# Optimization experiments

Measured on AMD Instinct MI355X. Metric: run time of the kernel, lower is better.

## Reference

```python
import jax, jax.numpy as jnp
import numpy as np

B, N, K, C = 8, 4096, 32, 128
HEAD_DIM = 64          # out_channels(512) // num_heads(8)
POS_DIM = HEAD_DIM // 2
D_THRESHOLD = 0.04


def setup_inputs() -> dict:
    key = jax.random.key(0)
    ks = jax.random.split(key, 16)

    def W(k, fi, fo):
        return (jax.random.normal(k, (fi, fo), jnp.float32) / np.sqrt(fi)).astype(jnp.float32)

    return {
        "center_xyz": jax.random.normal(ks[0], (B, N, 3), jnp.float32),
        "center_features": jax.random.normal(ks[1], (B, N, C), jnp.float32),
        "neighbor_xyz": jax.random.normal(ks[2], (B, N, K, 3), jnp.float32),
        "neighbor_features": jax.random.normal(ks[3], (B, N, K, C), jnp.float32),
        "phi_w": W(ks[4], C, HEAD_DIM),   "phi_b": jnp.zeros((HEAD_DIM,), jnp.float32),
        "theta_w": W(ks[5], C, HEAD_DIM), "theta_b": jnp.zeros((HEAD_DIM,), jnp.float32),
        "m1_w": W(ks[6], 3, POS_DIM),     "m1_b": jnp.zeros((POS_DIM,), jnp.float32),
        "m2_w": W(ks[7], 3, POS_DIM),     "m2_b": jnp.zeros((POS_DIM,), jnp.float32),
        "psi_w": W(ks[8], 2 * POS_DIM, 1), "psi_b": jnp.zeros((1,), jnp.float32),
        "z_w": W(ks[9], C, HEAD_DIM),     "z_b": jnp.zeros((HEAD_DIM,), jnp.float32),
    }


def reference(center_xyz, center_features, neighbor_xyz, neighbor_features,
              phi_w, phi_b, theta_w, theta_b, m1_w, m1_b, m2_w, m2_b,
              psi_w, psi_b, z_w, z_b):
    relu = jax.nn.relu
    # feature affinity r_f: (B,N,K,1)
    feat_i = relu(center_features @ phi_w + phi_b)        # (B,N,H)
    feat_j = relu(neighbor_features @ theta_w + theta_b)  # (B,N,K,H)
    r_f = jnp.sum(feat_i[:, :, None, :] * feat_j, axis=-1, keepdims=True)
    # positional score r_l_base: (B,N,K,1)
    pos_i = relu(center_xyz @ m1_w + m1_b)                # (B,N,P)
    pos_j = relu(neighbor_xyz @ m2_w + m2_b)              # (B,N,K,P)
    pos_i_t = jnp.broadcast_to(pos_i[:, :, None, :], pos_j.shape)
    r_l_base = relu(jnp.concatenate([pos_i_t, pos_j], axis=-1) @ psi_w + psi_b)
    # SPIL mask: same frame (z coord equal) AND distance > threshold
    t_i = center_xyz[..., 2][:, :, None]                  # (B,N,1)
    t_j = neighbor_xyz[..., 2]                            # (B,N,K)
    same_frame = (t_i == t_j).astype(jnp.float32)
    euclid = jnp.linalg.norm(center_xyz[:, :, None, :] - neighbor_xyz, axis=-1)
    dist_mask = (euclid > D_THRESHOLD).astype(jnp.float32)
    mask = same_frame * dist_mask                         # (B,N,K)
    r_l = r_l_base * (1.0 - mask[..., None])
    # masked, r_l-weighted softmax over K
    r_f = r_f / jnp.sqrt(jnp.float32(HEAD_DIM))
    r_f_max = jnp.max(r_f, axis=2, keepdims=True)
    numerator = r_l * jnp.exp(r_f - r_f_max)
    denominator = jnp.sum(numerator, axis=2, keepdims=True) + 1e-8
    W_ij = numerator / denominator                        # (B,N,K,1)
    transformed = neighbor_features @ z_w + z_b           # (B,N,K,H)
    return jnp.sum(W_ij * transformed, axis=2)            # (B,N,H)
```

## Files before the change

### kernel.cpp

```cpp
#include <hip/hip_runtime.h>
#include <hip/hip_bf16.h>


#define Bq 8
#define Nq 4096
#define Kq 32
#define Cq 128
#define Hq 64

typedef __bf16 bf16x8 __attribute__((ext_vector_type(8)));
typedef float  f32x4  __attribute__((ext_vector_type(4)));

__device__ __forceinline__ unsigned short f2bf(float f) {
  __hip_bfloat16 h = __float2bfloat16(f);
  return *reinterpret_cast<unsigned short*>(&h);
}
__device__ __forceinline__ float bf2f(unsigned short u) {
  return __uint_as_float(((unsigned int)u) << 16);
}

__global__ __launch_bounds__(256) void prep_w(const float* __restrict__ theta_w,
                                              const float* __restrict__ z_w,
                                              const float* __restrict__ phi_w,
                                              unsigned short* __restrict__ WcT,
                                              unsigned short* __restrict__ phiT) {
  int idx = blockIdx.x * 256 + threadIdx.x;
  if (idx < 16384) {
    int h = idx >> 7, c = idx & 127;
    float v = (h < 64) ? theta_w[c * 64 + h] : z_w[c * 64 + (h - 64)];
    WcT[idx] = f2bf(v);
  } else {
    int i2 = idx - 16384;
    int h = i2 >> 7, c = i2 & 127;
    phiT[i2] = f2bf(phi_w[c * 64 + h]);
  }
}

__global__ __launch_bounds__(256) void phi_gemm(
    const float* __restrict__ cf, const float* __restrict__ cxyz,
    const unsigned short* __restrict__ phiT, const float* __restrict__ phi_b,
    const float* __restrict__ m1_w, const float* __restrict__ m1_b,
    const float* __restrict__ psi_w,
    float* __restrict__ feat_out, float* __restrict__ s_out) {
  __shared__ __align__(16) unsigned short Xs[128 * 128];
  const int t = threadIdx.x;
  const int wave = t >> 6, lane = t & 63;
  const int lo16 = lane & 15, quad = lane >> 4;
  const size_t n0 = (size_t)blockIdx.x * 128;

  bf16x8 wf[4][4];
#pragma unroll
  for (int ks = 0; ks < 4; ks++)
#pragma unroll
    for (int nt = 0; nt < 4; nt++)
      wf[ks][nt] = *(const bf16x8*)(phiT + (size_t)(nt * 16 + lo16) * 128 + ks * 32 + quad * 8);

  const float4* xsrc = (const float4*)(cf + n0 * Cq);
  ushort4* xdst4 = (ushort4*)Xs;
#pragma unroll
  for (int i = 0; i < 16; i++) {
    int j = t + i * 256;
    float4 v = xsrc[j];
    int r = j >> 5, w = j & 31;
    int g = w >> 1, hf = w & 1;
    int p = g ^ (r & 15);
    ushort4 pk;
    pk.x = f2bf(v.x); pk.y = f2bf(v.y); pk.z = f2bf(v.z); pk.w = f2bf(v.w);
    xdst4[r * 32 + p * 2 + hf] = pk;
  }
  __syncthreads();

  f32x4 acc[2][4];
#pragma unroll
  for (int mt = 0; mt < 2; mt++)
#pragma unroll
    for (int nt = 0; nt < 4; nt++) acc[mt][nt] = (f32x4){0.f, 0.f, 0.f, 0.f};
#pragma unroll
  for (int ks = 0; ks < 4; ks++) {
    int p = (ks * 4 + quad) ^ lo16;
    bf16x8 a[2];
#pragma unroll
    for (int mt = 0; mt < 2; mt++) {
      int row = wave * 32 + mt * 16 + lo16;
      a[mt] = *(const bf16x8*)(Xs + row * 128 + p * 8);
    }
#pragma unroll
    for (int mt = 0; mt < 2; mt++)
#pragma unroll
      for (int nt = 0; nt < 4; nt++)
        acc[mt][nt] = __builtin_amdgcn_mfma_f32_16x16x32_bf16(a[mt], wf[ks][nt], acc[mt][nt], 0, 0, 0);
  }

#pragma unroll
  for (int mt = 0; mt < 2; mt++)
#pragma unroll
    for (int nt = 0; nt < 4; nt++) {
      int h = nt * 16 + lo16;
      float b = phi_b[h];
#pragma unroll
      for (int r = 0; r < 4; r++) {
        int row = wave * 32 + mt * 16 + quad * 4 + r;
        feat_out[(n0 + row) * 64 + h] = fmaxf(acc[mt][nt][r] + b, 0.f);
      }
    }

  if (t < 128) {
    size_t n = n0 + t;
    float x = cxyz[n * 3], y = cxyz[n * 3 + 1], z = cxyz[n * 3 + 2];
    float s = 0.f;
#pragma unroll 4
    for (int p = 0; p < 32; p++) {
      float pi = fmaxf(fmaf(x, m1_w[p], fmaf(y, m1_w[32 + p], fmaf(z, m1_w[64 + p], m1_b[p]))), 0.f);
      s = fmaf(pi, psi_w[p], s);
    }
    s_out[n] = s;
  }
}

__global__ __launch_bounds__(256, 3) void spil_main(
    const float* __restrict__ cxyz, const float* __restrict__ nxyz,
    const float* __restrict__ nf,
    const float* __restrict__ theta_b, const float* __restrict__ m2_w,
    const float* __restrict__ m2_b, const float* __restrict__ psi_w,
    const float* __restrict__ psi_b, const float* __restrict__ z_b,
    const unsigned short* __restrict__ WcT,
    const float* __restrict__ feat_i, const float* __restrict__ s_i,
    float* __restrict__ out) {
  __shared__ __align__(16) char smem[35968];
  unsigned short* Xs   = (unsigned short*)smem;
  unsigned short* outt = (unsigned short*)smem;
  float* feat_s = (float*)(smem + 33792);
  float* m2w_s  = feat_s + 256;
  float* m2b_s  = m2w_s + 96;
  float* psij_s = m2b_s + 32;
  float* zb_s   = psij_s + 32;
  float* tb_s   = zb_s + 64;

  const int t = threadIdx.x;
  const int wave = t >> 6, lane = t & 63;
  const int lo16 = lane & 15, quad = lane >> 4;
  const size_t n0 = (size_t)blockIdx.x * 4;

  const int mhalf = wave & 1, nhalf = wave >> 1;
  bf16x8 wf[4][4];
#pragma unroll
  for (int ks = 0; ks < 4; ks++)
#pragma unroll
    for (int nt = 0; nt < 4; nt++)
      wf[ks][nt] = *(const bf16x8*)(WcT + (size_t)(nhalf * 64 + nt * 16 + lo16) * 128 + ks * 32 + quad * 8);

  const float4* xsrc = (const float4*)(nf + n0 * Kq * Cq);
  ushort4* xdst4 = (ushort4*)Xs;
#pragma unroll
  for (int i = 0; i < 16; i++) {
    int j = t + i * 256;
    float4 v = xsrc[j];
    int r = j >> 5, w = j & 31;
    int g = w >> 1, hf = w & 1;
    int p = g ^ (r & 15);
    ushort4 pk;
    pk.x = f2bf(v.x); pk.y = f2bf(v.y); pk.z = f2bf(v.z); pk.w = f2bf(v.w);
    xdst4[r * 32 + p * 2 + hf] = pk;
  }
  __syncthreads();

  f32x4 acc[4][4];
#pragma unroll
  for (int mt = 0; mt < 4; mt++)
#pragma unroll
    for (int nt = 0; nt < 4; nt++) acc[mt][nt] = (f32x4){0.f, 0.f, 0.f, 0.f};
#pragma unroll
  for (int ks = 0; ks < 4; ks++) {
    int p = (ks * 4 + quad) ^ lo16;
    bf16x8 a[4];
#pragma unroll
    for (int mt = 0; mt < 4; mt++) {
      int row = mhalf * 64 + mt * 16 + lo16;
      a[mt] = *(const bf16x8*)(Xs + row * 128 + p * 8);
    }
#pragma unroll
    for (int mt = 0; mt < 4; mt++)
#pragma unroll
      for (int nt = 0; nt < 4; nt++)
        acc[mt][nt] = __builtin_amdgcn_mfma_f32_16x16x32_bf16(a[mt], wf[ks][nt], acc[mt][nt], 0, 0, 0);
  }
  __syncthreads();

#pragma unroll
  for (int mt = 0; mt < 4; mt++) {
    int row0 = mhalf * 64 + mt * 16 + quad * 4;
#pragma unroll
    for (int nt = 0; nt < 4; nt++) {
      int col = nhalf * 64 + nt * 16 + lo16;
#pragma unroll
      for (int r = 0; r < 4; r++)
        outt[(row0 + r) * 132 + col] = f2bf(acc[mt][nt][r]);
    }
  }
  feat_s[t] = feat_i[n0 * 64 + t];
  if (t < 96) m2w_s[t] = m2_w[t];
  if (t < 32) { m2b_s[t] = m2_b[t]; psij_s[t] = psi_w[32 + t]; }
  if (t < 64) { zb_s[t] = z_b[t]; tb_s[t] = theta_b[t]; }
  __syncthreads();

  const int nl = wave;
  const size_t ng = n0 + nl;
  const int k = lane & 31, half = lane >> 5;
  const int baser = nl * 32;

  const float* fi = feat_s + nl * 64;
  const unsigned short* orow = outt + (size_t)(baser + k) * 132;
  float v = 0.f;
#pragma unroll
  for (int i = 0; i < 32; i++) {
    int h = half * 32 + i;
    float fj = fmaxf(bf2f(orow[h]) + tb_s[h], 0.f);
    v = fmaf(fj, fi[h], v);
  }
  v += __shfl_xor(v, 32);
  float r_f = v * 0.125f;

  float cx = cxyz[ng * 3 + 0], cy = cxyz[ng * 3 + 1], cz = cxyz[ng * 3 + 2];
  const float* nxp = nxyz + (ng * Kq + (size_t)k) * 3;
  float xj = nxp[0], yj = nxp[1], zj = nxp[2];
  float sj = 0.f;
#pragma unroll
  for (int p = 0; p < 32; p++) {
    float pj = fmaxf(fmaf(xj, m2w_s[p], fmaf(yj, m2w_s[32 + p], fmaf(zj, m2w_s[64 + p], m2b_s[p]))), 0.f);
    sj = fmaf(pj, psij_s[p], sj);
  }
  float rl = fmaxf(s_i[ng] + sj + psi_b[0], 0.f);
  float dx = cx - xj, dy = cy - yj, dz = cz - zj;
  float dist = sqrtf(dx * dx + dy * dy + dz * dz);
  if (cz == zj && dist > 0.04f) rl = 0.f;

  float m = r_f;
#pragma unroll
  for (int off = 16; off; off >>= 1) m = fmaxf(m, __shfl_xor(m, off));
  float e = rl * __expf(r_f - m);
  float s = e;
#pragma unroll
  for (int off = 16; off; off >>= 1) s += __shfl_xor(s, off);
  float wgt = e / (s + 1e-8f);

  const int h = lane;
  const float zb = zb_s[h];
  float o = 0.f;
#pragma unroll
  for (int kk = 0; kk < 32; kk++) {
    float w = __shfl(wgt, kk);
    o = fmaf(w, bf2f(outt[(baser + kk) * 132 + 64 + h]) + zb, o);
  }
  out[ng * 64 + h] = o;
}

extern "C" void kernel_launch(void* const* d_in, const int* in_sizes, int n_in,
                              void* d_out, int out_size, void* d_ws, size_t ws_size,
                              hipStream_t stream) {
  const float* cxyz    = (const float*)d_in[0];
  const float* cf      = (const float*)d_in[1];
  const float* nxyz    = (const float*)d_in[2];
  const float* nf      = (const float*)d_in[3];
  const float* phi_w   = (const float*)d_in[4];
  const float* phi_b   = (const float*)d_in[5];
  const float* theta_w = (const float*)d_in[6];
  const float* theta_b = (const float*)d_in[7];
  const float* m1_w    = (const float*)d_in[8];
  const float* m1_b    = (const float*)d_in[9];
  const float* m2_w    = (const float*)d_in[10];
  const float* m2_b    = (const float*)d_in[11];
  const float* psi_w   = (const float*)d_in[12];
  const float* psi_b   = (const float*)d_in[13];
  const float* z_w     = (const float*)d_in[14];
  const float* z_b     = (const float*)d_in[15];
  float* outp = (float*)d_out;

  char* ws = (char*)d_ws;
  unsigned short* WcT  = (unsigned short*)ws;
  unsigned short* phiT = (unsigned short*)(ws + 32768);
  float* feat = (float*)(ws + 49152);
  float* s_i  = (float*)(ws + 49152 + (size_t)Bq * Nq * 64 * 4);

  prep_w<<<96, 256, 0, stream>>>(theta_w, z_w, phi_w, WcT, phiT);
  phi_gemm<<<(Bq * Nq) / 128, 256, 0, stream>>>(cf, cxyz, phiT, phi_b, m1_w, m1_b, psi_w, feat, s_i);
  spil_main<<<(Bq * Nq) / 4, 256, 0, stream>>>(cxyz, nxyz, nf, theta_b, m2_w, m2_b, psi_w, psi_b,
                                               z_b, WcT, feat, s_i, outp);
}
```

Before: 741.6 us.

## Make spil_main persistent over 8 tiles with double-buffered LDS prefetch

Each block now processes eight 4-point tiles in a loop instead of one. The weight fragments are loaded once per block, and the next tile's neighbor features are read from global into registers while the current tile's MFMA runs, then written into an alternate LDS buffer. This aims to hide global load latency and amortize the per-block weight loads. The costs are doubled LDS use (about 70KB), lower occupancy (launch bounds 2 instead of 3), higher register pressure from holding 16 prefetched ushort4 values, and a grid of only 1024 blocks.

```diff
diff --git a/kernel.cpp b/kernel.cpp
--- a/kernel.cpp
+++ b/kernel.cpp
@@ -7,6 +7,7 @@
 #define Kq 32
 #define Cq 128
 #define Hq 64
+#define TILES 8
 
 typedef __bf16 bf16x8 __attribute__((ext_vector_type(8)));
 typedef float  f32x4  __attribute__((ext_vector_type(4)));
@@ -117,7 +118,7 @@
   }
 }
 
-__global__ __launch_bounds__(256, 3) void spil_main(
+__global__ __launch_bounds__(256, 2) void spil_main(
     const float* __restrict__ cxyz, const float* __restrict__ nxyz,
     const float* __restrict__ nf,
     const float* __restrict__ theta_b, const float* __restrict__ m2_w,
@@ -126,11 +127,9 @@
     const unsigned short* __restrict__ WcT,
     const float* __restrict__ feat_i, const float* __restrict__ s_i,
     float* __restrict__ out) {
-  __shared__ __align__(16) char smem[35968];
-  unsigned short* Xs   = (unsigned short*)smem;
-  unsigned short* outt = (unsigned short*)smem;
-  float* feat_s = (float*)(smem + 33792);
-  float* m2w_s  = feat_s + 256;
+  __shared__ __align__(16) char smem[70784];
+  float* feat_d = (float*)(smem + 67584);
+  float* m2w_s  = feat_d + 512;
   float* m2b_s  = m2w_s + 96;
   float* psij_s = m2b_s + 32;
   float* zb_s   = psij_s + 32;
@@ -139,9 +138,9 @@
   const int t = threadIdx.x;
   const int wave = t >> 6, lane = t & 63;
   const int lo16 = lane & 15, quad = lane >> 4;
-  const size_t n0 = (size_t)blockIdx.x * 4;
-
   const int mhalf = wave & 1, nhalf = wave >> 1;
+  const size_t g0 = (size_t)blockIdx.x * TILES;
+
   bf16x8 wf[4][4];
 #pragma unroll
   for (int ks = 0; ks < 4; ks++)
@@ -149,109 +148,145 @@
     for (int nt = 0; nt < 4; nt++)
       wf[ks][nt] = *(const bf16x8*)(WcT + (size_t)(nhalf * 64 + nt * 16 + lo16) * 128 + ks * 32 + quad * 8);
 
-  const float4* xsrc = (const float4*)(nf + n0 * Kq * Cq);
-  ushort4* xdst4 = (ushort4*)Xs;
-#pragma unroll
-  for (int i = 0; i < 16; i++) {
-    int j = t + i * 256;
-    float4 v = xsrc[j];
-    int r = j >> 5, w = j & 31;
-    int g = w >> 1, hf = w & 1;
-    int p = g ^ (r & 15);
-    ushort4 pk;
-    pk.x = f2bf(v.x); pk.y = f2bf(v.y); pk.z = f2bf(v.z); pk.w = f2bf(v.w);
-    xdst4[r * 32 + p * 2 + hf] = pk;
-  }
-  __syncthreads();
-
-  f32x4 acc[4][4];
-#pragma unroll
-  for (int mt = 0; mt < 4; mt++)
-#pragma unroll
-    for (int nt = 0; nt < 4; nt++) acc[mt][nt] = (f32x4){0.f, 0.f, 0.f, 0.f};
-#pragma unroll
-  for (int ks = 0; ks < 4; ks++) {
-    int p = (ks * 4 + quad) ^ lo16;
-    bf16x8 a[4];
-#pragma unroll
-    for (int mt = 0; mt < 4; mt++) {
-      int row = mhalf * 64 + mt * 16 + lo16;
-      a[mt] = *(const bf16x8*)(Xs + row * 128 + p * 8);
-    }
-#pragma unroll
-    for (int mt = 0; mt < 4; mt++)
-#pragma unroll
-      for (int nt = 0; nt < 4; nt++)
-        acc[mt][nt] = __builtin_amdgcn_mfma_f32_16x16x32_bf16(a[mt], wf[ks][nt], acc[mt][nt], 0, 0, 0);
-  }
-  __syncthreads();
-
-#pragma unroll
-  for (int mt = 0; mt < 4; mt++) {
-    int row0 = mhalf * 64 + mt * 16 + quad * 4;
-#pragma unroll
-    for (int nt = 0; nt < 4; nt++) {
-      int col = nhalf * 64 + nt * 16 + lo16;
-#pragma unroll
-      for (int r = 0; r < 4; r++)
-        outt[(row0 + r) * 132 + col] = f2bf(acc[mt][nt][r]);
-    }
-  }
-  feat_s[t] = feat_i[n0 * 64 + t];
   if (t < 96) m2w_s[t] = m2_w[t];
   if (t < 32) { m2b_s[t] = m2_b[t]; psij_s[t] = psi_w[32 + t]; }
   if (t < 64) { zb_s[t] = z_b[t]; tb_s[t] = theta_b[t]; }
+
+  {
+    const float4* xsrc = (const float4*)(nf + g0 * 4 * Kq * Cq);
+    ushort4* xd = (ushort4*)smem;
+#pragma unroll
+    for (int i = 0; i < 16; i++) {
+      int j = t + i * 256;
+      float4 v = xsrc[j];
+      int r = j >> 5, w = j & 31;
+      int g = w >> 1, hf = w & 1;
+      int p = g ^ (r & 15);
+      ushort4 pk;
+      pk.x = f2bf(v.x); pk.y = f2bf(v.y); pk.z = f2bf(v.z); pk.w = f2bf(v.w);
+      xd[r * 32 + p * 2 + hf] = pk;
+    }
+    feat_d[t] = feat_i[g0 * 256 + t];
+  }
   __syncthreads();
 
-  const int nl = wave;
-  const size_t ng = n0 + nl;
-  const int k = lane & 31, half = lane >> 5;
-  const int baser = nl * 32;
-
-  const float* fi = feat_s + nl * 64;
-  const unsigned short* orow = outt + (size_t)(baser + k) * 132;
-  float v = 0.f;
-#pragma unroll
-  for (int i = 0; i < 32; i++) {
-    int h = half * 32 + i;
-    float fj = fmaxf(bf2f(orow[h]) + tb_s[h], 0.f);
-    v = fmaf(fj, fi[h], v);
-  }
-  v += __shfl_xor(v, 32);
-  float r_f = v * 0.125f;
-
-  float cx = cxyz[ng * 3 + 0], cy = cxyz[ng * 3 + 1], cz = cxyz[ng * 3 + 2];
-  const float* nxp = nxyz + (ng * Kq + (size_t)k) * 3;
-  float xj = nxp[0], yj = nxp[1], zj = nxp[2];
-  float sj = 0.f;
-#pragma unroll
-  for (int p = 0; p < 32; p++) {
-    float pj = fmaxf(fmaf(xj, m2w_s[p], fmaf(yj, m2w_s[32 + p], fmaf(zj, m2w_s[64 + p], m2b_s[p]))), 0.f);
-    sj = fmaf(pj, psij_s[p], sj);
-  }
-  float rl = fmaxf(s_i[ng] + sj + psi_b[0], 0.f);
-  float dx = cx - xj, dy = cy - yj, dz = cz - zj;
-  float dist = sqrtf(dx * dx + dy * dy + dz * dz);
-  if (cz == zj && dist > 0.04f) rl = 0.f;
-
-  float m = r_f;
-#pragma unroll
-  for (int off = 16; off; off >>= 1) m = fmaxf(m, __shfl_xor(m, off));
-  float e = rl * __expf(r_f - m);
-  float s = e;
-#pragma unroll
-  for (int off = 16; off; off >>= 1) s += __shfl_xor(s, off);
-  float wgt = e / (s + 1e-8f);
-
-  const int h = lane;
-  const float zb = zb_s[h];
-  float o = 0.f;
-#pragma unroll
-  for (int kk = 0; kk < 32; kk++) {
-    float w = __shfl(wgt, kk);
-    o = fmaf(w, bf2f(outt[(baser + kk) * 132 + 64 + h]) + zb, o);
-  }
-  out[ng * 64 + h] = o;
+  int cur = 0;
+  for (int it = 0; it < TILES; ++it) {
+    const size_t gtile = g0 + it;
+    const size_t n0 = gtile * 4;
+    const bool more = (it + 1 < TILES);
+
+    ushort4 pk[16];
+    if (more) {
+      const float4* xsrc = (const float4*)(nf + (n0 + 4) * Kq * Cq);
+#pragma unroll
+      for (int i = 0; i < 16; i++) {
+        float4 v = xsrc[t + i * 256];
+        pk[i].x = f2bf(v.x); pk[i].y = f2bf(v.y); pk[i].z = f2bf(v.z); pk[i].w = f2bf(v.w);
+      }
+    }
+
+    const size_t ng = n0 + wave;
+    const int k = lane & 31, half = lane >> 5;
+    const float* nxp = nxyz + (ng * Kq + (size_t)k) * 3;
+    const float xj = nxp[0], yj = nxp[1], zj = nxp[2];
+    const float cx = cxyz[ng * 3], cy = cxyz[ng * 3 + 1], cz = cxyz[ng * 3 + 2];
+    const float sI = s_i[ng];
+
+    const unsigned short* Xs = (const unsigned short*)(smem + cur * 33792);
+    f32x4 acc[4][4];
+#pragma unroll
+    for (int mt = 0; mt < 4; mt++)
+#pragma unroll
+      for (int nt = 0; nt < 4; nt++) acc[mt][nt] = (f32x4){0.f, 0.f, 0.f, 0.f};
+#pragma unroll
+    for (int ks = 0; ks < 4; ks++) {
+      int p = (ks * 4 + quad) ^ lo16;
+      bf16x8 a[4];
+#pragma unroll
+      for (int mt = 0; mt < 4; mt++) {
+        int row = mhalf * 64 + mt * 16 + lo16;
+        a[mt] = *(const bf16x8*)(Xs + row * 128 + p * 8);
+      }
+#pragma unroll
+      for (int mt = 0; mt < 4; mt++)
+#pragma unroll
+        for (int nt = 0; nt < 4; nt++)
+          acc[mt][nt] = __builtin_amdgcn_mfma_f32_16x16x32_bf16(a[mt], wf[ks][nt], acc[mt][nt], 0, 0, 0);
+    }
+    __syncthreads();
+
+    unsigned short* outt = (unsigned short*)(smem + cur * 33792);
+#pragma unroll
+    for (int mt = 0; mt < 4; mt++) {
+      int row0 = mhalf * 64 + mt * 16 + quad * 4;
+#pragma unroll
+      for (int nt = 0; nt < 4; nt++) {
+        int col = nhalf * 64 + nt * 16 + lo16;
+#pragma unroll
+        for (int r = 0; r < 4; r++)
+          outt[(row0 + r) * 132 + col] = f2bf(acc[mt][nt][r]);
+      }
+    }
+
+    if (more) {
+      ushort4* xd = (ushort4*)(smem + (cur ^ 1) * 33792);
+#pragma unroll
+      for (int i = 0; i < 16; i++) {
+        int j = t + i * 256;
+        int r = j >> 5, w = j & 31;
+        int g = w >> 1, hf = w & 1;
+        int p = g ^ (r & 15);
+        xd[r * 32 + p * 2 + hf] = pk[i];
+      }
+      feat_d[(cur ^ 1) * 256 + t] = feat_i[(gtile + 1) * 256 + t];
+    }
+    __syncthreads();
+
+    const float* fi = feat_d + cur * 256 + wave * 64;
+    const unsigned short* orow = outt + (size_t)(wave * 32 + k) * 132;
+    float vv = 0.f;
+#pragma unroll
+    for (int i = 0; i < 32; i++) {
+      int h = half * 32 + i;
+      float fj = fmaxf(bf2f(orow[h]) + tb_s[h], 0.f);
+      vv = fmaf(fj, fi[h], vv);
+    }
+    vv += __shfl_xor(vv, 32);
+    float r_f = vv * 0.125f;
+
+    float sj = 0.f;
+#pragma unroll
+    for (int p = 0; p < 32; p++) {
+      float pj = fmaxf(fmaf(xj, m2w_s[p], fmaf(yj, m2w_s[32 + p], fmaf(zj, m2w_s[64 + p], m2b_s[p]))), 0.f);
+      sj = fmaf(pj, psij_s[p], sj);
+    }
+    float rl = fmaxf(sI + sj + psi_b[0], 0.f);
+    float dx = cx - xj, dy = cy - yj, dz = cz - zj;
+    float dist = sqrtf(dx * dx + dy * dy + dz * dz);
+    if (cz == zj && dist > 0.04f) rl = 0.f;
+
+    float m = r_f;
+#pragma unroll
+    for (int off = 16; off; off >>= 1) m = fmaxf(m, __shfl_xor(m, off));
+    float e = rl * __expf(r_f - m);
+    float s = e;
+#pragma unroll
+    for (int off = 16; off; off >>= 1) s += __shfl_xor(s, off);
+    float wgt = e / (s + 1e-8f);
+
+    const int h = lane;
+    const float zb = zb_s[h];
+    float o = 0.f;
+#pragma unroll
+    for (int kk = 0; kk < 32; kk++) {
+      float w = __shfl(wgt, kk);
+      o = fmaf(w, bf2f(outt[(wave * 32 + kk) * 132 + 64 + h]) + zb, o);
+    }
+    out[ng * 64 + h] = o;
+
+    cur ^= 1;
+  }
 }
 
 extern "C" void kernel_launch(void* const* d_in, const int* in_sizes, int n_in,
@@ -283,6 +318,6 @@
 
   prep_w<<<96, 256, 0, stream>>>(theta_w, z_w, phi_w, WcT, phiT);
   phi_gemm<<<(Bq * Nq) / 128, 256, 0, stream>>>(cf, cxyz, phiT, phi_b, m1_w, m1_b, psi_w, feat, s_i);
-  spil_main<<<(Bq * Nq) / 4, 256, 0, stream>>>(cxyz, nxyz, nf, theta_b, m2_w, m2_b, psi_w, psi_b,
-                                               z_b, WcT, feat, s_i, outp);
-}
+  spil_main<<<(Bq * Nq) / 4 / TILES, 256, 0, stream>>>(cxyz, nxyz, nf, theta_b, m2_w, m2_b, psi_w,
+                                                       psi_b, z_b, WcT, feat, s_i, outp);
+}
```

New measurement: 790.4 us. +6.6%, slower.

## Fuse center-feature phi projection and center positional score into main kernel

Applied to the files above, without the earlier changes.

Removes the separate phi_gemm kernel and its workspace round-trip for feat_i and s_i. The main kernel now loads the four center feature rows into shared memory and computes the phi projection in fp32 with scalar FMAs, reading phi_w from global memory. It also computes the center positional score with a wave shuffle reduction. This trades one kernel launch and the intermediate global traffic for extra per-block scalar work and more shared memory.

```diff
diff --git a/kernel.cpp b/kernel.cpp
--- a/kernel.cpp
+++ b/kernel.cpp
@@ -21,41 +21,53 @@
 
 __global__ __launch_bounds__(256) void prep_w(const float* __restrict__ theta_w,
                                               const float* __restrict__ z_w,
-                                              const float* __restrict__ phi_w,
-                                              unsigned short* __restrict__ WcT,
-                                              unsigned short* __restrict__ phiT) {
+                                              unsigned short* __restrict__ WcT) {
   int idx = blockIdx.x * 256 + threadIdx.x;
-  if (idx < 16384) {
-    int h = idx >> 7, c = idx & 127;
-    float v = (h < 64) ? theta_w[c * 64 + h] : z_w[c * 64 + (h - 64)];
-    WcT[idx] = f2bf(v);
-  } else {
-    int i2 = idx - 16384;
-    int h = i2 >> 7, c = i2 & 127;
-    phiT[i2] = f2bf(phi_w[c * 64 + h]);
-  }
-}
-
-__global__ __launch_bounds__(256) void phi_gemm(
-    const float* __restrict__ cf, const float* __restrict__ cxyz,
-    const unsigned short* __restrict__ phiT, const float* __restrict__ phi_b,
+  int h = idx >> 7, c = idx & 127;
+  float v = (h < 64) ? theta_w[c * 64 + h] : z_w[c * 64 + (h - 64)];
+  WcT[idx] = f2bf(v);
+}
+
+__global__ __launch_bounds__(256, 3) void spil_main(
+    const float* __restrict__ cxyz, const float* __restrict__ nxyz,
+    const float* __restrict__ nf, const float* __restrict__ cf,
+    const float* __restrict__ phi_w, const float* __restrict__ phi_b,
+    const float* __restrict__ theta_b,
     const float* __restrict__ m1_w, const float* __restrict__ m1_b,
-    const float* __restrict__ psi_w,
-    float* __restrict__ feat_out, float* __restrict__ s_out) {
-  __shared__ __align__(16) unsigned short Xs[128 * 128];
+    const float* __restrict__ m2_w, const float* __restrict__ m2_b,
+    const float* __restrict__ psi_w, const float* __restrict__ psi_b,
+    const float* __restrict__ z_b,
+    const unsigned short* __restrict__ WcT,
+    float* __restrict__ out) {
+  __shared__ __align__(16) char smem[38656];
+  unsigned short* Xs   = (unsigned short*)smem;
+  unsigned short* outt = (unsigned short*)smem;
+  float* base   = (float*)(smem + 33792);
+  float* feat_s = base;
+  float* m2w_s  = base + 256;
+  float* m2b_s  = base + 352;
+  float* psij_s = base + 384;
+  float* zb_s   = base + 416;
+  float* tb_s   = base + 480;
+  float* m1w_s  = base + 544;
+  float* m1b_s  = base + 640;
+  float* psii_s = base + 672;
+  float* cf_s   = base + 704;
+
   const int t = threadIdx.x;
   const int wave = t >> 6, lane = t & 63;
   const int lo16 = lane & 15, quad = lane >> 4;
-  const size_t n0 = (size_t)blockIdx.x * 128;
-
+  const size_t n0 = (size_t)blockIdx.x * 4;
+
+  const int mhalf = wave & 1, nhalf = wave >> 1;
   bf16x8 wf[4][4];
 #pragma unroll
   for (int ks = 0; ks < 4; ks++)
 #pragma unroll
     for (int nt = 0; nt < 4; nt++)
-      wf[ks][nt] = *(const bf16x8*)(phiT + (size_t)(nt * 16 + lo16) * 128 + ks * 32 + quad * 8);
-
-  const float4* xsrc = (const float4*)(cf + n0 * Cq);
+      wf[ks][nt] = *(const bf16x8*)(WcT + (size_t)(nhalf * 64 + nt * 16 + lo16) * 128 + ks * 32 + quad * 8);
+
+  const float4* xsrc = (const float4*)(nf + n0 * Kq * Cq);
   ushort4* xdst4 = (ushort4*)Xs;
 #pragma unroll
   for (int i = 0; i < 16; i++) {
@@ -68,100 +80,11 @@
     pk.x = f2bf(v.x); pk.y = f2bf(v.y); pk.z = f2bf(v.z); pk.w = f2bf(v.w);
     xdst4[r * 32 + p * 2 + hf] = pk;
   }
-  __syncthreads();
-
-  f32x4 acc[2][4];
-#pragma unroll
-  for (int mt = 0; mt < 2; mt++)
-#pragma unroll
-    for (int nt = 0; nt < 4; nt++) acc[mt][nt] = (f32x4){0.f, 0.f, 0.f, 0.f};
-#pragma unroll
-  for (int ks = 0; ks < 4; ks++) {
-    int p = (ks * 4 + quad) ^ lo16;
-    bf16x8 a[2];
-#pragma unroll
-    for (int mt = 0; mt < 2; mt++) {
-      int row = wave * 32 + mt * 16 + lo16;
-      a[mt] = *(const bf16x8*)(Xs + row * 128 + p * 8);
-    }
-#pragma unroll
-    for (int mt = 0; mt < 2; mt++)
-#pragma unroll
-      for (int nt = 0; nt < 4; nt++)
-        acc[mt][nt] = __builtin_amdgcn_mfma_f32_16x16x32_bf16(a[mt], wf[ks][nt], acc[mt][nt], 0, 0, 0);
-  }
-
-#pragma unroll
-  for (int mt = 0; mt < 2; mt++)
-#pragma unroll
-    for (int nt = 0; nt < 4; nt++) {
-      int h = nt * 16 + lo16;
-      float b = phi_b[h];
-#pragma unroll
-      for (int r = 0; r < 4; r++) {
-        int row = wave * 32 + mt * 16 + quad * 4 + r;
-        feat_out[(n0 + row) * 64 + h] = fmaxf(acc[mt][nt][r] + b, 0.f);
-      }
-    }
-
-  if (t < 128) {
-    size_t n = n0 + t;
-    float x = cxyz[n * 3], y = cxyz[n * 3 + 1], z = cxyz[n * 3 + 2];
-    float s = 0.f;
-#pragma unroll 4
-    for (int p = 0; p < 32; p++) {
-      float pi = fmaxf(fmaf(x, m1_w[p], fmaf(y, m1_w[32 + p], fmaf(z, m1_w[64 + p], m1_b[p]))), 0.f);
-      s = fmaf(pi, psi_w[p], s);
-    }
-    s_out[n] = s;
-  }
-}
-
-__global__ __launch_bounds__(256, 3) void spil_main(
-    const float* __restrict__ cxyz, const float* __restrict__ nxyz,
-    const float* __restrict__ nf,
-    const float* __restrict__ theta_b, const float* __restrict__ m2_w,
-    const float* __restrict__ m2_b, const float* __restrict__ psi_w,
-    const float* __restrict__ psi_b, const float* __restrict__ z_b,
-    const unsigned short* __restrict__ WcT,
-    const float* __restrict__ feat_i, const float* __restrict__ s_i,
-    float* __restrict__ out) {
-  __shared__ __align__(16) char smem[35968];
-  unsigned short* Xs   = (unsigned short*)smem;
-  unsigned short* outt = (unsigned short*)smem;
-  float* feat_s = (float*)(smem + 33792);
-  float* m2w_s  = feat_s + 256;
-  float* m2b_s  = m2w_s + 96;
-  float* psij_s = m2b_s + 32;
-  float* zb_s   = psij_s + 32;
-  float* tb_s   = zb_s + 64;
-
-  const int t = threadIdx.x;
-  const int wave = t >> 6, lane = t & 63;
-  const int lo16 = lane & 15, quad = lane >> 4;
-  const size_t n0 = (size_t)blockIdx.x * 4;
-
-  const int mhalf = wave & 1, nhalf = wave >> 1;
-  bf16x8 wf[4][4];
-#pragma unroll
-  for (int ks = 0; ks < 4; ks++)
-#pragma unroll
-    for (int nt = 0; nt < 4; nt++)
-      wf[ks][nt] = *(const bf16x8*)(WcT + (size_t)(nhalf * 64 + nt * 16 + lo16) * 128 + ks * 32 + quad * 8);
-
-  const float4* xsrc = (const float4*)(nf + n0 * Kq * Cq);
-  ushort4* xdst4 = (ushort4*)Xs;
-#pragma unroll
-  for (int i = 0; i < 16; i++) {
-    int j = t + i * 256;
-    float4 v = xsrc[j];
-    int r = j >> 5, w = j & 31;
-    int g = w >> 1, hf = w & 1;
-    int p = g ^ (r & 15);
-    ushort4 pk;
-    pk.x = f2bf(v.x); pk.y = f2bf(v.y); pk.z = f2bf(v.z); pk.w = f2bf(v.w);
-    xdst4[r * 32 + p * 2 + hf] = pk;
-  }
+  if (t < 96) { m2w_s[t] = m2_w[t]; m1w_s[t] = m1_w[t]; }
+  if (t < 32) { m2b_s[t] = m2_b[t]; psij_s[t] = psi_w[32 + t];
+                m1b_s[t] = m1_b[t]; psii_s[t] = psi_w[t]; }
+  if (t < 64) { zb_s[t] = z_b[t]; tb_s[t] = theta_b[t]; }
+  if (t < 128) ((float4*)cf_s)[t] = ((const float4*)(cf + n0 * Cq))[t];
   __syncthreads();
 
   f32x4 acc[4][4];
@@ -197,18 +120,32 @@
         outt[(row0 + r) * 132 + col] = f2bf(acc[mt][nt][r]);
     }
   }
-  feat_s[t] = feat_i[n0 * 64 + t];
-  if (t < 96) m2w_s[t] = m2_w[t];
-  if (t < 32) { m2b_s[t] = m2_b[t]; psij_s[t] = psi_w[32 + t]; }
-  if (t < 64) { zb_s[t] = z_b[t]; tb_s[t] = theta_b[t]; }
+
+  {
+    const float* cfrow = cf_s + wave * 128;
+    float f = phi_b[lane];
+#pragma unroll 8
+    for (int c = 0; c < 128; c++)
+      f = fmaf(cfrow[c], phi_w[c * 64 + lane], f);
+    feat_s[wave * 64 + lane] = fmaxf(f, 0.f);
+  }
+
+  const size_t ng = n0 + wave;
+  const float cx = cxyz[ng * 3], cy = cxyz[ng * 3 + 1], cz = cxyz[ng * 3 + 2];
+  float sI;
+  {
+    int p = lane & 31;
+    float pi = fmaxf(fmaf(cx, m1w_s[p], fmaf(cy, m1w_s[32 + p], fmaf(cz, m1w_s[64 + p], m1b_s[p]))), 0.f);
+    sI = pi * psii_s[p];
+#pragma unroll
+    for (int off = 16; off; off >>= 1) sI += __shfl_xor(sI, off);
+  }
   __syncthreads();
 
-  const int nl = wave;
-  const size_t ng = n0 + nl;
   const int k = lane & 31, half = lane >> 5;
-  const int baser = nl * 32;
-
-  const float* fi = feat_s + nl * 64;
+  const int baser = wave * 32;
+
+  const float* fi = feat_s + wave * 64;
   const unsigned short* orow = outt + (size_t)(baser + k) * 132;
   float v = 0.f;
 #pragma unroll
@@ -220,7 +157,6 @@
   v += __shfl_xor(v, 32);
   float r_f = v * 0.125f;
 
-  float cx = cxyz[ng * 3 + 0], cy = cxyz[ng * 3 + 1], cz = cxyz[ng * 3 + 2];
   const float* nxp = nxyz + (ng * Kq + (size_t)k) * 3;
   float xj = nxp[0], yj = nxp[1], zj = nxp[2];
   float sj = 0.f;
@@ -229,7 +165,7 @@
     float pj = fmaxf(fmaf(xj, m2w_s[p], fmaf(yj, m2w_s[32 + p], fmaf(zj, m2w_s[64 + p], m2b_s[p]))), 0.f);
     sj = fmaf(pj, psij_s[p], sj);
   }
-  float rl = fmaxf(s_i[ng] + sj + psi_b[0], 0.f);
+  float rl = fmaxf(sI + sj + psi_b[0], 0.f);
   float dx = cx - xj, dy = cy - yj, dz = cz - zj;
   float dist = sqrtf(dx * dx + dy * dy + dz * dz);
   if (cz == zj && dist > 0.04f) rl = 0.f;
@@ -275,14 +211,10 @@
   const float* z_b     = (const float*)d_in[15];
   float* outp = (float*)d_out;
 
-  char* ws = (char*)d_ws;
-  unsigned short* WcT  = (unsigned short*)ws;
-  unsigned short* phiT = (unsigned short*)(ws + 32768);
-  float* feat = (float*)(ws + 49152);
-  float* s_i  = (float*)(ws + 49152 + (size_t)Bq * Nq * 64 * 4);
-
-  prep_w<<<96, 256, 0, stream>>>(theta_w, z_w, phi_w, WcT, phiT);
-  phi_gemm<<<(Bq * Nq) / 128, 256, 0, stream>>>(cf, cxyz, phiT, phi_b, m1_w, m1_b, psi_w, feat, s_i);
-  spil_main<<<(Bq * Nq) / 4, 256, 0, stream>>>(cxyz, nxyz, nf, theta_b, m2_w, m2_b, psi_w, psi_b,
-                                               z_b, WcT, feat, s_i, outp);
-}
+  unsigned short* WcT = (unsigned short*)d_ws;
+
+  prep_w<<<64, 256, 0, stream>>>(theta_w, z_w, WcT);
+  spil_main<<<(Bq * Nq) / 4, 256, 0, stream>>>(cxyz, nxyz, nf, cf, phi_w, phi_b, theta_b,
+                                               m1_w, m1_b, m2_w, m2_b, psi_w, psi_b, z_b,
+                                               WcT, outp);
+}
```

After: 801.7 us. 1.08x slower.
